# Optimization experiments

Measured on AMD Instinct MI355X. Metric: run time of the kernel, lower is better.

The kernel has to match this reference:

```python
import math
import jax, jax.numpy as jnp
import numpy as np

C = 1024
H = 16
HD = C // H
T = 2048
B = 2
EPS = 1e-5


def setup_inputs() -> dict:
    key = jax.random.key(0)
    ks = jax.random.split(key, 8)
    s = 0.02
    return {
        "x": jax.random.normal(ks[0], (B, T, C), dtype=jnp.float32),
        "ln1_g": jnp.ones((C,), jnp.float32),
        "ln1_b": jnp.zeros((C,), jnp.float32),
        "w_attn": jax.random.normal(ks[1], (C, 3 * C), dtype=jnp.float32) * s,
        "b_attn": jnp.zeros((3 * C,), jnp.float32),
        "w_proj": jax.random.normal(ks[2], (C, C), dtype=jnp.float32) * s,
        "b_proj": jnp.zeros((C,), jnp.float32),
        "ln2_g": jnp.ones((C,), jnp.float32),
        "ln2_b": jnp.zeros((C,), jnp.float32),
        "w_fc": jax.random.normal(ks[3], (C, 4 * C), dtype=jnp.float32) * s,
        "b_fc": jnp.zeros((4 * C,), jnp.float32),
        "w_fc2": jax.random.normal(ks[4], (4 * C, C), dtype=jnp.float32) * s,
        "b_fc2": jnp.zeros((C,), jnp.float32),
    }


def _layernorm(x, g, b):
    mu = jnp.mean(x, axis=-1, keepdims=True)
    var = jnp.mean((x - mu) ** 2, axis=-1, keepdims=True)
    return (x - mu) * jax.lax.rsqrt(var + EPS) * g + b


def _attention(x, w_attn, b_attn, w_proj, b_proj):
    Bb, Tt, Cc = x.shape
    qkv = x @ w_attn + b_attn  # (B,T,3C)
    q, k, v = jnp.split(qkv, 3, axis=-1)
    # (B,H,T,HD)
    q = q.reshape(Bb, Tt, H, HD).transpose(0, 2, 1, 3)
    k = k.reshape(Bb, Tt, H, HD).transpose(0, 2, 1, 3)
    v = v.reshape(Bb, Tt, H, HD).transpose(0, 2, 1, 3)
    scale = 1.0 / math.sqrt(HD)
    attn = jnp.einsum("bhqd,bhkd->bhqk", q, k) * scale
    causal = jnp.tril(jnp.ones((Tt, Tt), dtype=bool))
    attn = jnp.where(causal[None, None], attn, -jnp.inf)
    attn = jax.nn.softmax(attn, axis=-1)
    out = jnp.einsum("bhqk,bhkd->bhqd", attn, v)
    out = out.transpose(0, 2, 1, 3).reshape(Bb, Tt, Cc)
    return out @ w_proj + b_proj


def _mlp(x, w_fc, b_fc, w_fc2, b_fc2):
    h = jax.nn.gelu(x @ w_fc + b_fc, approximate=True)
    return h @ w_fc2 + b_fc2


def reference(x, ln1_g, ln1_b, w_attn, b_attn, w_proj, b_proj,
              ln2_g, ln2_b, w_fc, b_fc, w_fc2, b_fc2):
    x = x + _attention(_layernorm(x, ln1_g, ln1_b), w_attn, b_attn, w_proj, b_proj)
    x = x + _mlp(_layernorm(x, ln2_g, ln2_b), w_fc, b_fc, w_fc2, b_fc2)
    return x
```

## Files before the change

### kernel.cpp

```cpp
#include <hip/hip_runtime.h>
#include <math.h>

#define TB 2
#define TT 2048
#define TC 1024
#define TH 16
#define THD 64
#define TM (TB*TT)
#define NQT 32

typedef __bf16 bf16x8 __attribute__((ext_vector_type(8)));
typedef float f32x4 __attribute__((ext_vector_type(4)));
typedef unsigned short u16x8 __attribute__((ext_vector_type(8)));
typedef unsigned short u16x4 __attribute__((ext_vector_type(4)));

__device__ __forceinline__ unsigned short f2bf(float f){
    unsigned int u = __builtin_bit_cast(unsigned int, f);
    u = (u + 0x7FFFu + ((u >> 16) & 1u)) >> 16;
    return (unsigned short)u;
}
__device__ __forceinline__ float bf2f(unsigned short h){
    unsigned int u = ((unsigned int)h) << 16;
    return __builtin_bit_cast(float, u);
}
__device__ __forceinline__ bf16x8 ldbf8(const unsigned short* p){
    return __builtin_bit_cast(bf16x8, *(const u16x8*)p);
}
__device__ __forceinline__ void gl_lds16(const void* g, void* l){
    __builtin_amdgcn_global_load_lds(
        (const __attribute__((address_space(1))) unsigned int*)g,
        (__attribute__((address_space(3))) unsigned int*)l,
        16, 0, 0);
}
__device__ __forceinline__ float gelu_tanh(float v){
    float u = 2.0f * 0.7978845608028654f * (v + 0.044715f * v * v * v);
    u = fminf(fmaxf(u, -30.f), 30.f);
    float e = __expf(u);
    return 0.5f * v * (1.f + (e - 1.f) / (e + 1.f));
}

__global__ __launch_bounds__(256)
void prep_all(const float* __restrict__ w_attn, const float* __restrict__ w_proj,
              const float* __restrict__ w_fc,   const float* __restrict__ w_fc2,
              unsigned short* __restrict__ wattnT, unsigned short* __restrict__ wprojT,
              unsigned short* __restrict__ wfcT,   unsigned short* __restrict__ wfc2T,
              const float* __restrict__ x, const float* __restrict__ ln1_g,
              const float* __restrict__ ln1_b, unsigned short* __restrict__ xn1){
    const int bid = blockIdx.x;
    const int t = threadIdx.x;
    if (bid >= 12288){
        const int row = bid - 12288;
        const float4* xr = (const float4*)(x + (size_t)row * TC);
        float4 v = xr[t];
        float s  = v.x + v.y + v.z + v.w;
        float s2 = v.x*v.x + v.y*v.y + v.z*v.z + v.w*v.w;
        #pragma unroll
        for (int off = 32; off; off >>= 1){
            s  += __shfl_down(s,  off);
            s2 += __shfl_down(s2, off);
        }
        __shared__ float red[8];
        int l = t & 63, wv = t >> 6;
        if (l == 0){ red[wv] = s; red[4 + wv] = s2; }
        __syncthreads();
        float S  = red[0] + red[1] + red[2] + red[3];
        float S2 = red[4] + red[5] + red[6] + red[7];
        float mu = S * (1.f / TC);
        float var = S2 * (1.f / TC) - mu * mu;
        float rs = rsqrtf(var + 1e-5f);
        int c = t * 4;
        float4 gg = *(const float4*)(ln1_g + c);
        float4 bb = *(const float4*)(ln1_b + c);
        u16x4 o;
        o[0] = f2bf((v.x - mu) * rs * gg.x + bb.x);
        o[1] = f2bf((v.y - mu) * rs * gg.y + bb.y);
        o[2] = f2bf((v.z - mu) * rs * gg.z + bb.z);
        o[3] = f2bf((v.w - mu) * rs * gg.w + bb.w);
        *(u16x4*)(xn1 + (size_t)row * TC + c) = o;
        return;
    }
    __shared__ float tile[32][33];
    const float* in; unsigned short* out; int K, N, bx, by;
    if (bid < 3072)      { in=w_attn; out=wattnT; K=1024; N=3072; bx=bid%96;  by=bid/96; }
    else if (bid < 4096) { int lo=bid-3072; in=w_proj; out=wprojT; K=1024; N=1024; bx=lo%32;  by=lo/32; }
    else if (bid < 8192) { int lo=bid-4096; in=w_fc;   out=wfcT;   K=1024; N=4096; bx=lo%128; by=lo/128; }
    else                 { int lo=bid-8192; in=w_fc2;  out=wfc2T;  K=4096; N=1024; bx=lo%32;  by=lo/32; }
    int tx = t & 31, ty = t >> 5;
    int n0 = bx * 32, k0 = by * 32;
    #pragma unroll
    for (int i = 0; i < 4; i++)
        tile[ty + 8*i][tx] = in[(size_t)(k0 + ty + 8*i) * N + n0 + tx];
    __syncthreads();
    #pragma unroll
    for (int i = 0; i < 4; i++)
        out[(size_t)(n0 + ty + 8*i) * K + k0 + tx] = f2bf(tile[tx][ty + 8*i]);
}

__global__ __launch_bounds__(256)
void ln_kernel(const float* __restrict__ x, const float* __restrict__ g,
               const float* __restrict__ be, unsigned short* __restrict__ y){
    const int row = blockIdx.x, t = threadIdx.x;
    const float4* xr = (const float4*)(x + (size_t)row * TC);
    float4 v = xr[t];
    float s  = v.x + v.y + v.z + v.w;
    float s2 = v.x*v.x + v.y*v.y + v.z*v.z + v.w*v.w;
    #pragma unroll
    for (int off = 32; off; off >>= 1){
        s  += __shfl_down(s,  off);
        s2 += __shfl_down(s2, off);
    }
    __shared__ float red[8];
    int l = t & 63, wv = t >> 6;
    if (l == 0){ red[wv] = s; red[4 + wv] = s2; }
    __syncthreads();
    float S  = red[0] + red[1] + red[2] + red[3];
    float S2 = red[4] + red[5] + red[6] + red[7];
    float mu = S * (1.f / TC);
    float var = S2 * (1.f / TC) - mu * mu;
    float rs = rsqrtf(var + 1e-5f);
    int c = t * 4;
    float4 gg = *(const float4*)(g + c);
    float4 bb = *(const float4*)(be + c);
    u16x4 o;
    o[0] = f2bf((v.x - mu) * rs * gg.x + bb.x);
    o[1] = f2bf((v.y - mu) * rs * gg.y + bb.y);
    o[2] = f2bf((v.z - mu) * rs * gg.z + bb.z);
    o[3] = f2bf((v.w - mu) * rs * gg.w + bb.w);
    *(u16x4*)(y + (size_t)row * TC + c) = o;
}

template<int EPI>
__global__ __launch_bounds__(256, 2)
void gemm_bt(const unsigned short* __restrict__ A,
             const unsigned short* __restrict__ Bt,
             const float* __restrict__ bias,
             const float* __restrict__ resid,
             void* __restrict__ outv,
             int M, int N, int K){
    __shared__ unsigned short lA[128 * 32];
    __shared__ unsigned short lB[128 * 32];
    const int t = threadIdx.x, w = t >> 6, l = t & 63, lr = l & 15, lg = l >> 4;
    const int nt = N >> 7;
    const int nwg = gridDim.x;
    const int bid = blockIdx.x;
    int wg = (nwg & 7) ? bid : ((bid & 7) * (nwg >> 3) + (bid >> 3));
    const int bm = wg / nt, bn = wg % nt;
    const int row0 = bm << 7, col0 = bn << 7;
    const int wr = w >> 1, wc = w & 1;

    f32x4 acc[4][4];
    #pragma unroll
    for (int i = 0; i < 4; i++)
        #pragma unroll
        for (int j = 0; j < 4; j++) acc[i][j] = (f32x4){0.f,0.f,0.f,0.f};

    const char* Ag = (const char*)(A + (size_t)(row0 + (t >> 2)) * K) + (t & 3) * 16;
    const char* Bg = (const char*)(Bt + (size_t)(col0 + (t >> 2)) * K) + (t & 3) * 16;
    const size_t rstep = (size_t)64 * K * 2;
    char* lAw = (char*)lA + w * 1024;
    char* lBw = (char*)lB + w * 1024;

    for (int k0 = 0; k0 < K; k0 += 32){
        size_t kb = (size_t)k0 * 2;
        gl_lds16(Ag + kb,          lAw);
        gl_lds16(Ag + kb + rstep,  lAw + 4096);
        gl_lds16(Bg + kb,          lBw);
        gl_lds16(Bg + kb + rstep,  lBw + 4096);
        __syncthreads();
        bf16x8 af[4], bfr[4];
        #pragma unroll
        for (int mi = 0; mi < 4; mi++)
            af[mi] = ldbf8(lA + (wr*64 + mi*16 + lr) * 32 + lg * 8);
        #pragma unroll
        for (int ni = 0; ni < 4; ni++)
            bfr[ni] = ldbf8(lB + (wc*64 + ni*16 + lr) * 32 + lg * 8);
        #pragma unroll
        for (int mi = 0; mi < 4; mi++)
            #pragma unroll
            for (int ni = 0; ni < 4; ni++)
                acc[mi][ni] = __builtin_amdgcn_mfma_f32_16x16x32_bf16(
                    af[mi], bfr[ni], acc[mi][ni], 0, 0, 0);
        __syncthreads();
    }

    float bcol[4];
    #pragma unroll
    for (int ni = 0; ni < 4; ni++) bcol[ni] = bias[col0 + wc*64 + ni*16 + lr];
    #pragma unroll
    for (int mi = 0; mi < 4; mi++){
        #pragma unroll
        for (int j = 0; j < 4; j++){
            int row = row0 + wr*64 + mi*16 + lg*4 + j;
            size_t base = (size_t)row * N + col0 + wc*64 + lr;
            #pragma unroll
            for (int ni = 0; ni < 4; ni++){
                float v = acc[mi][ni][j] + bcol[ni];
                size_t idx = base + (size_t)ni * 16;
                if (EPI == 0)      ((unsigned short*)outv)[idx] = f2bf(v);
                else if (EPI == 1) ((float*)outv)[idx] = v + resid[idx];
                else               ((unsigned short*)outv)[idx] = f2bf(gelu_tanh(v));
            }
        }
    }
}

template<int MH>
__device__ __forceinline__ void gloadA(const unsigned short* bufA, bf16x8 (&af)[4][2],
                                       int wm, int lr, int sl0, int sl1){
    #pragma unroll
    for (int i = 0; i < 4; i++){
        int lrow = (wm*128 + (MH*4 + i)*16 + lr) * 64;
        af[i][0] = ldbf8(bufA + lrow + sl0);
        af[i][1] = ldbf8(bufA + lrow + sl1);
    }
}
__device__ __forceinline__ void gloadB(const unsigned short* bufB, bf16x8 (&bfr)[4][2],
                                       int wn, int lr, int sl0, int sl1){
    #pragma unroll
    for (int i = 0; i < 4; i++){
        int brow = (wn*64 + i*16 + lr) * 64;
        bfr[i][0] = ldbf8(bufB + brow + sl0);
        bfr[i][1] = ldbf8(bufB + brow + sl1);
    }
}
template<int MH, int NH>
__device__ __forceinline__ void gmma(const bf16x8 (&af)[4][2], const bf16x8 (&bfr)[4][2],
                                     f32x4 (&acc)[8][4]){
    #pragma unroll
    for (int i = 0; i < 4; i++)
        #pragma unroll
        for (int j = 0; j < 2; j++){
            f32x4& a = acc[MH*4 + i][NH*2 + j];
            a = __builtin_amdgcn_mfma_f32_16x16x32_bf16(af[i][0], bfr[NH*2+j][0], a, 0,0,0);
            a = __builtin_amdgcn_mfma_f32_16x16x32_bf16(af[i][1], bfr[NH*2+j][1], a, 0,0,0);
        }
}

#define G256_LOOP(NT_, KBEG_)                                                   \
    for (int tk = 0; tk < (NT_); ++tk){                                         \
        const int cur = tk & 1;                                                 \
        const bool more = (tk + 1) < (NT_);                                     \
        const unsigned short* bufA = &lds[cur][0][0];                           \
        const unsigned short* bufB = &lds[cur][1][0];                           \
        if (more){                                                              \
            stage(cur ^ 1, (KBEG_) + (tk + 1)*64, 0);                           \
            asm volatile("s_waitcnt vmcnt(2)" ::: "memory");                    \
        } else {                                                                \
            asm volatile("s_waitcnt vmcnt(0)" ::: "memory");                    \
        }                                                                       \
        __builtin_amdgcn_s_barrier();                                           \
        bf16x8 af[4][2], bfr[4][2];                                             \
        gloadA<0>(bufA, af, wm, lr, sl0, sl1);                                  \
        gloadB(bufB, bfr, wn, lr, sl0, sl1);                                    \
        if (more) stage(cur ^ 1, (KBEG_) + (tk + 1)*64, 1);                     \
        __builtin_amdgcn_s_barrier();                                           \
        asm volatile("s_waitcnt lgkmcnt(0)" ::: "memory");                      \
        __builtin_amdgcn_sched_barrier(0);                                      \
        __builtin_amdgcn_s_setprio(1);                                          \
        gmma<0,0>(af, bfr, acc);                                                \
        __builtin_amdgcn_s_setprio(0);                                          \
        __builtin_amdgcn_s_barrier();                                           \
        if (more) stage(cur ^ 1, (KBEG_) + (tk + 1)*64, 2);                     \
        __builtin_amdgcn_s_setprio(1);                                          \
        gmma<0,1>(af, bfr, acc);                                                \
        __builtin_amdgcn_s_setprio(0);                                          \
        __builtin_amdgcn_s_barrier();                                           \
        gloadA<1>(bufA, af, wm, lr, sl0, sl1);                                  \
        if (more) stage(cur ^ 1, (KBEG_) + (tk + 1)*64, 3);                     \
        __builtin_amdgcn_s_barrier();                                           \
        asm volatile("s_waitcnt lgkmcnt(0)" ::: "memory");                      \
        __builtin_amdgcn_sched_barrier(0);                                      \
        __builtin_amdgcn_s_setprio(1);                                          \
        gmma<1,0>(af, bfr, acc);                                                \
        __builtin_amdgcn_s_setprio(0);                                          \
        __builtin_amdgcn_s_barrier();                                           \
        __builtin_amdgcn_s_setprio(1);                                          \
        gmma<1,1>(af, bfr, acc);                                                \
        __builtin_amdgcn_s_setprio(0);                                          \
        __builtin_amdgcn_s_barrier();                                           \
    }

template<int EPI>
__global__ __launch_bounds__(512, 1)
void gemm256(const unsigned short* __restrict__ A,
             const unsigned short* __restrict__ Bt,
             const float* __restrict__ bias,
             void* __restrict__ outv,
             int M, int N, int K){
    __shared__ unsigned short lds[2][2][256*64];
    const int t = threadIdx.x;
    const int w = t >> 6, l = t & 63, lr = l & 15, lg = l >> 4;
    const int wm = w >> 2, wn = w & 3;
    const int lr7 = lr & 7;
    const int sl0 = (lg ^ lr7) << 3;
    const int sl1 = ((4 + lg) ^ lr7) << 3;
    const int nbn = N >> 8;
    const int nwg = (M >> 8) * nbn;
    const int bid = blockIdx.x;
    const int wg = (nwg & 7) ? bid : ((bid & 7) * (nwg >> 3) + (bid >> 3));
    const int bm = wg / nbn, bn = wg % nbn;
    const size_t row0 = (size_t)bm << 8, col0 = (size_t)bn << 8;
    const int NT = K >> 6;

    f32x4 acc[8][4];
    #pragma unroll
    for (int i = 0; i < 8; i++)
        #pragma unroll
        for (int j = 0; j < 4; j++) acc[i][j] = (f32x4){0.f,0.f,0.f,0.f};

    int rowc[4], slogc[4];
    #pragma unroll
    for (int c = 0; c < 4; c++){
        int seg = t + (c << 9);
        rowc[c]  = seg >> 3;
        slogc[c] = (((seg & 7) ^ ((seg >> 3) & 7)) << 3);
    }
    const unsigned short* Abase = A  + row0 * K;
    const unsigned short* Bbase = Bt + col0 * K;
    auto stage = [&](int buf, int kofs, int c){
        int seg = t + (c << 9);
        const unsigned short* sa = Abase + (size_t)rowc[c] * K + kofs + slogc[c];
        const unsigned short* sb = Bbase + (size_t)rowc[c] * K + kofs + slogc[c];
        gl_lds16(sa, (void*)&lds[buf][0][seg * 8]);
        gl_lds16(sb, (void*)&lds[buf][1][seg * 8]);
    };

    #pragma unroll
    for (int c = 0; c < 4; c++) stage(0, 0, c);

    G256_LOOP(NT, 0)

    float bcol[4];
    #pragma unroll
    for (int ni = 0; ni < 4; ni++) bcol[ni] = bias[col0 + wn*64 + ni*16 + lr];
    unsigned short* outp = (unsigned short*)outv;
    #pragma unroll
    for (int mi = 0; mi < 8; mi++){
        #pragma unroll
        for (int j = 0; j < 4; j++){
            size_t row = row0 + wm*128 + mi*16 + lg*4 + j;
            size_t base = row * N + col0 + wn*64 + lr;
            #pragma unroll
            for (int ni = 0; ni < 4; ni++){
                float v = acc[mi][ni][j] + bcol[ni];
                size_t idx = base + (size_t)ni * 16;
                if (EPI == 0) outp[idx] = f2bf(v);
                else          outp[idx] = f2bf(gelu_tanh(v));
            }
        }
    }
}

__global__ __launch_bounds__(512, 1)
void gemm256sk(const unsigned short* __restrict__ A,
               const unsigned short* __restrict__ Bt,
               unsigned short* __restrict__ pout,
               int M, int N, int K, int klen){
    __shared__ unsigned short lds[2][2][256*64];
    const int t = threadIdx.x;
    const int w = t >> 6, l = t & 63, lr = l & 15, lg = l >> 4;
    const int wm = w >> 2, wn = w & 3;
    const int lr7 = lr & 7;
    const int sl0 = (lg ^ lr7) << 3;
    const int sl1 = ((4 + lg) ^ lr7) << 3;
    const int nbn = N >> 8;
    const int ntile = (M >> 8) * nbn;
    const int nwg = gridDim.x;
    const int bid = blockIdx.x;
    int wg = (nwg & 7) ? bid : ((bid & 7) * (nwg >> 3) + (bid >> 3));
    const int kh = wg / ntile;
    wg -= kh * ntile;
    const int bm = wg / nbn, bn = wg % nbn;
    const size_t row0 = (size_t)bm << 8, col0 = (size_t)bn << 8;
    const int NT = klen >> 6;
    const int kbeg = kh * klen;

    f32x4 acc[8][4];
    #pragma unroll
    for (int i = 0; i < 8; i++)
        #pragma unroll
        for (int j = 0; j < 4; j++) acc[i][j] = (f32x4){0.f,0.f,0.f,0.f};

    int rowc[4], slogc[4];
    #pragma unroll
    for (int c = 0; c < 4; c++){
        int seg = t + (c << 9);
        rowc[c]  = seg >> 3;
        slogc[c] = (((seg & 7) ^ ((seg >> 3) & 7)) << 3);
    }
    const unsigned short* Abase = A  + row0 * K;
    const unsigned short* Bbase = Bt + col0 * K;
    auto stage = [&](int buf, int kofs, int c){
        int seg = t + (c << 9);
        const unsigned short* sa = Abase + (size_t)rowc[c] * K + kofs + slogc[c];
        const unsigned short* sb = Bbase + (size_t)rowc[c] * K + kofs + slogc[c];
        gl_lds16(sa, (void*)&lds[buf][0][seg * 8]);
        gl_lds16(sb, (void*)&lds[buf][1][seg * 8]);
    };

    #pragma unroll
    for (int c = 0; c < 4; c++) stage(0, kbeg, c);

    G256_LOOP(NT, kbeg)

    unsigned short* outp = pout + (size_t)kh * M * N;
    #pragma unroll
    for (int mi = 0; mi < 8; mi++){
        #pragma unroll
        for (int j = 0; j < 4; j++){
            size_t row = row0 + wm*128 + mi*16 + lg*4 + j;
            size_t base = row * N + col0 + wn*64 + lr;
            #pragma unroll
            for (int ni = 0; ni < 4; ni++)
                outp[base + (size_t)ni * 16] = f2bf(acc[mi][ni][j]);
        }
    }
}

__global__ __launch_bounds__(256)
void combine_k4(const unsigned short* __restrict__ p,
                const float* __restrict__ bias, const float* __restrict__ resid,
                float* __restrict__ out){
    const size_t PS = (size_t)TM * TC;
    const int total = TM * TC / 4;
    for (int i = blockIdx.x * 256 + threadIdx.x; i < total; i += gridDim.x * 256){
        int e = i * 4;
        u16x4 a0 = *(const u16x4*)(p + e);
        u16x4 a1 = *(const u16x4*)(p + PS + e);
        u16x4 a2 = *(const u16x4*)(p + 2*PS + e);
        u16x4 a3 = *(const u16x4*)(p + 3*PS + e);
        float4 r = *(const float4*)(resid + e);
        float4 bb = *(const float4*)(bias + (e & (TC - 1)));
        float4 o;
        o.x = bf2f(a0[0]) + bf2f(a1[0]) + bf2f(a2[0]) + bf2f(a3[0]) + r.x + bb.x;
        o.y = bf2f(a0[1]) + bf2f(a1[1]) + bf2f(a2[1]) + bf2f(a3[1]) + r.y + bb.y;
        o.z = bf2f(a0[2]) + bf2f(a1[2]) + bf2f(a2[2]) + bf2f(a3[2]) + r.z + bb.z;
        o.w = bf2f(a0[3]) + bf2f(a1[3]) + bf2f(a2[3]) + bf2f(a3[3]) + r.w + bb.w;
        *(float4*)(out + e) = o;
    }
}

__global__ __launch_bounds__(256)
void vtrans(const unsigned short* __restrict__ qkv, unsigned short* __restrict__ vTg){
    __shared__ unsigned short lt[64][68];
    int kt = blockIdx.x & (NQT - 1);
    int bh = blockIdx.x >> 5;
    int h = bh & (TH - 1), b = bh >> 4;
    int t = threadIdx.x;
    int r = t >> 2, c4 = t & 3;
    const unsigned short* src = qkv + (size_t)(b*TT + kt*64 + r) * (3*TC) + 2*TC + h*THD;
    u16x8 a0 = *(const u16x8*)(src + c4*8);
    u16x8 a1 = *(const u16x8*)(src + 32 + c4*8);
    #pragma unroll
    for (int j = 0; j < 8; j++){
        lt[r][c4*8 + j]      = a0[j];
        lt[r][32 + c4*8 + j] = a1[j];
    }
    __syncthreads();
    int d = t >> 2;
    unsigned short* dst = vTg + ((size_t)bh * NQT + kt) * (64*80) + (size_t)d * 80;
    u16x8 o0, o1;
    #pragma unroll
    for (int j = 0; j < 8; j++){
        o0[j] = lt[c4*8 + j][d];
        o1[j] = lt[32 + c4*8 + j][d];
    }
    *(u16x8*)(dst + c4*8)      = o0;
    *(u16x8*)(dst + 32 + c4*8) = o1;
}

__global__ __launch_bounds__(256, 3)
void attn_kernel(const unsigned short* __restrict__ qkv,
                 const unsigned short* __restrict__ vTg,
                 unsigned short* __restrict__ attn_out){
    __shared__ unsigned short kbuf[128*64];
    __shared__ unsigned short vbuf[128*64];
    __shared__ unsigned short pl[4][16*136];

    const int bid = blockIdx.x;
    const int qrank = bid >> 5;
    const int bh = bid & 31;
    const int h = bh & (TH - 1), b = bh >> 4;
    const int qb = 31 - qrank;
    const int q0 = qb << 6;
    const int t = threadIdx.x, w = t >> 6, l = t & 63, lr = l & 15, lg = l >> 4;
    const int lr7 = lr & 7;
    const int sl0 = (lg ^ lr7) << 3;
    const int sl1 = ((4 + lg) ^ lr7) << 3;
    const float SC = 0.18033688011112042f;

    const int NP = (qb >> 1) + 1;
    const int qrow_base = q0 + w*16;
    const int myq = qrow_base + lr;

    const unsigned short* kgp[4];
    const unsigned short* vgp[4];
    #pragma unroll
    for (int p = 0; p < 4; p++){
        int vt = p*256 + t;
        int r  = vt >> 3;
        int sc = ((vt & 7) ^ (r & 7)) * 8;
        kgp[p] = qkv + (size_t)(b*TT + r) * (3*TC) + TC + h*THD + sc;
        vgp[p] = vTg + (size_t)bh * (NQT*64*80)
               + (size_t)(r >> 6) * (64*80) + (size_t)(r & 63) * 80 + sc;
    }
    const size_t kstep2 = (size_t)128 * (3*TC);
    const size_t vstep2 = (size_t)2 * (64*80);

    auto stage = [&](int pi){
        #pragma unroll
        for (int p = 0; p < 4; p++)
            gl_lds16(kgp[p] + (size_t)pi*kstep2, (void*)&kbuf[(p*256 + t)*8]);
        #pragma unroll
        for (int p = 0; p < 4; p++)
            gl_lds16(vgp[p] + (size_t)pi*vstep2, (void*)&vbuf[(p*256 + t)*8]);
    };

    const unsigned short* qr =
        qkv + (size_t)(b*TT + myq) * (3*TC) + h*THD;
    bf16x8 q0f = ldbf8(qr + lg*8), q1f = ldbf8(qr + 32 + lg*8);

    bf16x8 ones;
    #pragma unroll
    for (int i = 0; i < 8; i++) ones[i] = (__bf16)1.0f;

    f32x4 o[5];
    float m = -1e30f;
    #pragma unroll
    for (int i = 0; i < 5; i++) o[i] = (f32x4){0.f,0.f,0.f,0.f};

    unsigned short* plw = &pl[w][0];

    stage(0);
    for (int pi = 0; pi < NP; ++pi){
        const int t0 = 2*pi, t1 = 2*pi + 1;
        asm volatile("s_waitcnt vmcnt(0)" ::: "memory");
        __builtin_amdgcn_s_barrier();

        f32x4 s[8];
        __builtin_amdgcn_s_setprio(1);
        #pragma unroll
        for (int cb = 0; cb < 8; cb++){
            bf16x8 ka = ldbf8(kbuf + (cb*16 + lr)*64 + sl0);
            bf16x8 kbf = ldbf8(kbuf + (cb*16 + lr)*64 + sl1);
            f32x4 z = (f32x4){0.f,0.f,0.f,0.f};
            z = __builtin_amdgcn_mfma_f32_16x16x32_bf16(ka, q0f, z, 0,0,0);
            z = __builtin_amdgcn_mfma_f32_16x16x32_bf16(kbf, q1f, z, 0,0,0);
            s[cb] = z;
        }
        __builtin_amdgcn_s_setprio(0);
        if (t0 == qb){
            #pragma unroll
            for (int cb = 0; cb < 4; cb++)
                #pragma unroll
                for (int j = 0; j < 4; j++)
                    if (t0*64 + cb*16 + lg*4 + j > myq) s[cb][j] = -1e30f;
        }
        if (t1 == qb){
            #pragma unroll
            for (int cb = 4; cb < 8; cb++)
                #pragma unroll
                for (int j = 0; j < 4; j++)
                    if (t1*64 + (cb-4)*16 + lg*4 + j > myq) s[cb][j] = -1e30f;
        } else if (t1 > qb){
            #pragma unroll
            for (int cb = 4; cb < 8; cb++)
                #pragma unroll
                for (int j = 0; j < 4; j++) s[cb][j] = -1e30f;
        }
        float mloc = s[0][0];
        #pragma unroll
        for (int cb = 0; cb < 8; cb++)
            #pragma unroll
            for (int j = 0; j < 4; j++) mloc = fmaxf(mloc, s[cb][j]);
        mloc = fmaxf(mloc, __shfl_xor(mloc, 16));
        mloc = fmaxf(mloc, __shfl_xor(mloc, 32));
        bool grow = (mloc * SC > m);
        float al = 1.f;
        if (__any(grow)){
            float mn = fmaxf(m, mloc * SC);
            al = exp2f(m - mn);
            m = mn;
            float alb[4];
            #pragma unroll
            for (int j = 0; j < 4; j++) alb[j] = __shfl(al, lg*4 + j);
            #pragma unroll
            for (int db = 0; db < 5; db++)
                #pragma unroll
                for (int j = 0; j < 4; j++) o[db][j] *= alb[j];
        }
        #pragma unroll
        for (int cb = 0; cb < 8; cb++){
            u16x4 pk;
            #pragma unroll
            for (int j = 0; j < 4; j++){
                float e = exp2f(__builtin_fmaf(s[cb][j], SC, -m));
                pk[j] = f2bf(e);
            }
            *(u16x4*)(plw + lr*136 + cb*16 + lg*4) = pk;
        }
        bf16x8 pa0 = ldbf8(plw + lr*136 + lg*8);
        bf16x8 pa1 = ldbf8(plw + lr*136 + 32 + lg*8);
        bf16x8 pa2 = ldbf8(plw + lr*136 + 64 + lg*8);
        bf16x8 pa3 = ldbf8(plw + lr*136 + 96 + lg*8);
        __builtin_amdgcn_s_setprio(1);
        #pragma unroll
        for (int db = 0; db < 4; db++){
            bf16x8 v0a = ldbf8(vbuf + (db*16 + lr)*64 + sl0);
            bf16x8 v0b = ldbf8(vbuf + (db*16 + lr)*64 + sl1);
            o[db] = __builtin_amdgcn_mfma_f32_16x16x32_bf16(pa0, v0a, o[db], 0,0,0);
            o[db] = __builtin_amdgcn_mfma_f32_16x16x32_bf16(pa1, v0b, o[db], 0,0,0);
            bf16x8 v1a = ldbf8(vbuf + (64 + db*16 + lr)*64 + sl0);
            bf16x8 v1b = ldbf8(vbuf + (64 + db*16 + lr)*64 + sl1);
            o[db] = __builtin_amdgcn_mfma_f32_16x16x32_bf16(pa2, v1a, o[db], 0,0,0);
            o[db] = __builtin_amdgcn_mfma_f32_16x16x32_bf16(pa3, v1b, o[db], 0,0,0);
        }
        o[4] = __builtin_amdgcn_mfma_f32_16x16x32_bf16(pa0, ones, o[4], 0,0,0);
        o[4] = __builtin_amdgcn_mfma_f32_16x16x32_bf16(pa1, ones, o[4], 0,0,0);
        o[4] = __builtin_amdgcn_mfma_f32_16x16x32_bf16(pa2, ones, o[4], 0,0,0);
        o[4] = __builtin_amdgcn_mfma_f32_16x16x32_bf16(pa3, ones, o[4], 0,0,0);
        __builtin_amdgcn_s_setprio(0);

        __builtin_amdgcn_s_barrier();
        if (pi + 1 < NP) stage(pi + 1);
    }

    __bf16* aout = (__bf16*)attn_out;
    #pragma unroll
    for (int j = 0; j < 4; j++){
        float inv = 1.f / o[4][j];
        size_t tok = (size_t)(b*TT + qrow_base + lg*4 + j);
        #pragma unroll
        for (int db = 0; db < 4; db++)
            aout[tok*TC + h*THD + db*16 + lr] = (__bf16)(o[db][j] * inv);
    }
}

extern "C" void kernel_launch(void* const* d_in, const int* in_sizes, int n_in,
                              void* d_out, int out_size, void* d_ws, size_t ws_size,
                              hipStream_t stream){
    const float* x      = (const float*)d_in[0];
    const float* ln1_g  = (const float*)d_in[1];
    const float* ln1_b  = (const float*)d_in[2];
    const float* w_attn = (const float*)d_in[3];
    const float* b_attn = (const float*)d_in[4];
    const float* w_proj = (const float*)d_in[5];
    const float* b_proj = (const float*)d_in[6];
    const float* ln2_g  = (const float*)d_in[7];
    const float* ln2_b  = (const float*)d_in[8];
    const float* w_fc   = (const float*)d_in[9];
    const float* b_fc   = (const float*)d_in[10];
    const float* w_fc2  = (const float*)d_in[11];
    const float* b_fc2  = (const float*)d_in[12];
    float* out = (float*)d_out;

    char* ws = (char*)d_ws;
    size_t off = 0;
    auto alloc = [&](size_t bytes) -> void* {
        void* p = ws + off;
        off += (bytes + 255) & ~(size_t)255;
        return p;
    };
    unsigned short* wattnT = (unsigned short*)alloc((size_t)3072*1024*2);
    unsigned short* wprojT = (unsigned short*)alloc((size_t)1024*1024*2);
    unsigned short* wfcT   = (unsigned short*)alloc((size_t)4096*1024*2);
    unsigned short* wfc2T  = (unsigned short*)alloc((size_t)1024*4096*2);
    unsigned short* xn1    = (unsigned short*)alloc((size_t)TM*TC*2);
    unsigned short* qkvb   = (unsigned short*)alloc((size_t)TM*3*TC*2);
    float*          resid1 = (float*)alloc((size_t)TM*TC*4);
    unsigned short* xn2    = (unsigned short*)alloc((size_t)TM*TC*2);
    unsigned short* hbuf   = (unsigned short*)alloc((size_t)TM*4*TC*2);
    unsigned short* attnO  = (unsigned short*)alloc((size_t)TM*TC*2);
    unsigned short* vTg    = (unsigned short*)alloc((size_t)TB*TH*NQT*64*80*2);

    unsigned short* pks = xn1;

    prep_all<<<12288 + TM, 256, 0, stream>>>(
        w_attn, w_proj, w_fc, w_fc2, wattnT, wprojT, wfcT, wfc2T,
        x, ln1_g, ln1_b, xn1);

    gemm256<0><<<(TM/256)*(3072/256), 512, 0, stream>>>(
        xn1, wattnT, b_attn, qkvb, TM, 3072, 1024);

    vtrans<<<TB*TH*NQT, 256, 0, stream>>>(qkvb, vTg);

    attn_kernel<<<TB*TH*NQT, 256, 0, stream>>>(qkvb, vTg, attnO);

    gemm_bt<1><<<(TM/128)*(1024/128), 256, 0, stream>>>(
        attnO, wprojT, b_proj, x, resid1, TM, 1024, 1024);

    ln_kernel<<<TM, 256, 0, stream>>>(resid1, ln2_g, ln2_b, xn2);

    gemm256<2><<<(TM/256)*(4096/256), 512, 0, stream>>>(
        xn2, wfcT, b_fc, hbuf, TM, 4096, 1024);

    gemm256sk<<<4*(TM/256)*(1024/256), 512, 0, stream>>>(
        hbuf, wfc2T, pks, TM, 1024, 4096, 1024);
    combine_k4<<<2048, 256, 0, stream>>>(pks, b_fc2, resid1, out);
}
```

Before: 220.3 us.

## Restructure the 256x256 GEMM main loop to cut barriers and prefetch deeper

Rewrites the double-buffered GEMM loop so each k-tile uses two workgroup barriers instead of seven. The explicit lgkmcnt waits and sched_barriers between MFMA groups are dropped, so the compiler can interleave LDS reads with MFMAs. The first chunk of tile tk+2 is now issued into the just-freed buffer at the end of each iteration, and the prologue primes one extra chunk. This is meant to cut barrier stalls and hide more global-to-LDS latency, but it gives up manual control of the instruction schedule.

New measurement: 215.0 us, median of 3. -2.4%, faster.

```diff
diff --git a/kernel.cpp b/kernel.cpp
--- a/kernel.cpp
+++ b/kernel.cpp
@@ -239,45 +239,34 @@
 #define G256_LOOP(NT_, KBEG_)                                                   \
     for (int tk = 0; tk < (NT_); ++tk){                                         \
         const int cur = tk & 1;                                                 \
-        const bool more = (tk + 1) < (NT_);                                     \
+        const bool more1 = (tk + 1) < (NT_);                                    \
+        const bool more2 = (tk + 2) < (NT_);                                    \
         const unsigned short* bufA = &lds[cur][0][0];                           \
         const unsigned short* bufB = &lds[cur][1][0];                           \
-        if (more){                                                              \
-            stage(cur ^ 1, (KBEG_) + (tk + 1)*64, 0);                           \
-            asm volatile("s_waitcnt vmcnt(2)" ::: "memory");                    \
-        } else {                                                                \
-            asm volatile("s_waitcnt vmcnt(0)" ::: "memory");                    \
+        if (more1) asm volatile("s_waitcnt vmcnt(2)" ::: "memory");             \
+        else       asm volatile("s_waitcnt vmcnt(0)" ::: "memory");             \
+        __builtin_amdgcn_s_barrier();                                           \
+        {                                                                       \
+            bf16x8 afr[4][2], bfr[4][2];                                        \
+            gloadA<0>(bufA, afr, wm, lr, sl0, sl1);                             \
+            gloadB(bufB, bfr, wn, lr, sl0, sl1);                                \
+            if (more1){                                                         \
+                stage(cur ^ 1, (KBEG_) + (tk + 1)*64, 1);                       \
+                stage(cur ^ 1, (KBEG_) + (tk + 1)*64, 2);                       \
+            }                                                                   \
+            __builtin_amdgcn_s_setprio(1);                                      \
+            gmma<0,0>(afr, bfr, acc);                                           \
+            gmma<0,1>(afr, bfr, acc);                                           \
+            __builtin_amdgcn_s_setprio(0);                                      \
+            gloadA<1>(bufA, afr, wm, lr, sl0, sl1);                             \
+            if (more1) stage(cur ^ 1, (KBEG_) + (tk + 1)*64, 3);                \
+            __builtin_amdgcn_s_setprio(1);                                      \
+            gmma<1,0>(afr, bfr, acc);                                           \
+            gmma<1,1>(afr, bfr, acc);                                           \
+            __builtin_amdgcn_s_setprio(0);                                      \
         }                                                                       \
         __builtin_amdgcn_s_barrier();                                           \
-        bf16x8 af[4][2], bfr[4][2];                                             \
-        gloadA<0>(bufA, af, wm, lr, sl0, sl1);                                  \
-        gloadB(bufB, bfr, wn, lr, sl0, sl1);                                    \
-        if (more) stage(cur ^ 1, (KBEG_) + (tk + 1)*64, 1);                     \
-        __builtin_amdgcn_s_barrier();                                           \
-        asm volatile("s_waitcnt lgkmcnt(0)" ::: "memory");                      \
-        __builtin_amdgcn_sched_barrier(0);                                      \
-        __builtin_amdgcn_s_setprio(1);                                          \
-        gmma<0,0>(af, bfr, acc);                                                \
-        __builtin_amdgcn_s_setprio(0);                                          \
-        __builtin_amdgcn_s_barrier();                                           \
-        if (more) stage(cur ^ 1, (KBEG_) + (tk + 1)*64, 2);                     \
-        __builtin_amdgcn_s_setprio(1);                                          \
-        gmma<0,1>(af, bfr, acc);                                                \
-        __builtin_amdgcn_s_setprio(0);                                          \
-        __builtin_amdgcn_s_barrier();                                           \
-        gloadA<1>(bufA, af, wm, lr, sl0, sl1);                                  \
-        if (more) stage(cur ^ 1, (KBEG_) + (tk + 1)*64, 3);                     \
-        __builtin_amdgcn_s_barrier();                                           \
-        asm volatile("s_waitcnt lgkmcnt(0)" ::: "memory");                      \
-        __builtin_amdgcn_sched_barrier(0);                                      \
-        __builtin_amdgcn_s_setprio(1);                                          \
-        gmma<1,0>(af, bfr, acc);                                                \
-        __builtin_amdgcn_s_setprio(0);                                          \
-        __builtin_amdgcn_s_barrier();                                           \
-        __builtin_amdgcn_s_setprio(1);                                          \
-        gmma<1,1>(af, bfr, acc);                                                \
-        __builtin_amdgcn_s_setprio(0);                                          \
-        __builtin_amdgcn_s_barrier();                                           \
+        if (more2) stage(cur, (KBEG_) + (tk + 2)*64, 0);                        \
     }
 
 template<int EPI>
@@ -327,6 +316,7 @@
 
     #pragma unroll
     for (int c = 0; c < 4; c++) stage(0, 0, c);
+    if (NT > 1) stage(1, 64, 0);
 
     G256_LOOP(NT, 0)
 
@@ -400,6 +390,7 @@
 
     #pragma unroll
     for (int c = 0; c < 4; c++) stage(0, kbeg, c);
+    if (NT > 1) stage(1, kbeg + 64, 0);
 
     G256_LOOP(NT, kbeg)
 
```
